# Kernel tuning notes

Hardware: AMD Instinct MI355X
Metric: run time of the kernel (lower is better)

Reference implementation:

```python
import jax, jax.numpy as jnp
import numpy as np

EPS = np.finfo(np.float32).eps
X_DIM, H_DIM, Z_DIM = 256, 1024, 128
T, B = 128, 256

def _lin(key, fan_in, fan_out):
    k1, k2 = jax.random.split(key)
    lim = 1.0 / np.sqrt(fan_in)
    W = jax.random.uniform(k1, (fan_in, fan_out), jnp.float32, -lim, lim)
    b = jax.random.uniform(k2, (fan_out,), jnp.float32, -lim, lim)
    return W, b

def setup_inputs() -> dict:
    key = jax.random.key(0)
    ks = jax.random.split(key, 20)
    inp = {}
    inp['x'] = jax.random.normal(ks[0], (T, B, X_DIM), jnp.float32)
    inp['h'] = jnp.zeros((1, B, H_DIM), jnp.float32)
    inp['eps'] = jax.random.normal(ks[1], (T, B, Z_DIM), jnp.float32)
    inp['Wpx'], inp['bpx'] = _lin(ks[2], X_DIM, H_DIM)
    inp['Wpz'], inp['bpz'] = _lin(ks[3], Z_DIM, H_DIM)
    inp['Wenc'], inp['benc'] = _lin(ks[4], 2 * H_DIM, H_DIM)
    inp['Wem'], inp['bem'] = _lin(ks[5], H_DIM, Z_DIM)
    inp['Wes'], inp['bes'] = _lin(ks[6], H_DIM, Z_DIM)
    inp['Wpr'], inp['bpr'] = _lin(ks[7], H_DIM, H_DIM)
    inp['Wpm'], inp['bpm'] = _lin(ks[8], H_DIM, Z_DIM)
    inp['Wps'], inp['bps'] = _lin(ks[9], H_DIM, Z_DIM)
    inp['Wdec'], inp['bdec'] = _lin(ks[10], 2 * H_DIM, H_DIM)
    inp['Wdm'], inp['bdm'] = _lin(ks[11], H_DIM, X_DIM)
    inp['Wds'], inp['bds'] = _lin(ks[12], H_DIM, X_DIM)
    # GRU (pytorch layout): W_ih [3H, 2H], W_hh [3H, H]
    lim = 1.0 / np.sqrt(H_DIM)
    inp['W_ih'] = jax.random.uniform(ks[13], (3 * H_DIM, 2 * H_DIM), jnp.float32, -lim, lim)
    inp['W_hh'] = jax.random.uniform(ks[14], (3 * H_DIM, H_DIM), jnp.float32, -lim, lim)
    inp['b_ih'] = jax.random.uniform(ks[15], (3 * H_DIM,), jnp.float32, -lim, lim)
    inp['b_hh'] = jax.random.uniform(ks[16], (3 * H_DIM,), jnp.float32, -lim, lim)
    return inp

def reference(x, h, eps, Wpx, bpx, Wpz, bpz, Wenc, benc, Wem, bem, Wes, bes,
              Wpr, bpr, Wpm, bpm, Wps, bps, Wdec, bdec, Wdm, bdm, Wds, bds,
              W_ih, W_hh, b_ih, b_hh):
    relu = jax.nn.relu
    sp = jax.nn.softplus

    def gru_cell(inp, h_prev):
        gi = inp @ W_ih.T + b_ih          # [B, 3H]
        gh = h_prev @ W_hh.T + b_hh       # [B, 3H]
        i_r, i_z, i_n = jnp.split(gi, 3, axis=-1)
        h_r, h_z, h_n = jnp.split(gh, 3, axis=-1)
        r = jax.nn.sigmoid(i_r + h_r)
        u = jax.nn.sigmoid(i_z + h_z)
        n = jnp.tanh(i_n + r * h_n)
        return (1.0 - u) * n + u * h_prev

    def step(h_t, xe):
        x_t, eps_t = xe
        phi_x_t = relu(x_t @ Wpx + bpx)                               # [B,H]
        enc_t = relu(jnp.concatenate([phi_x_t, h_t], axis=1) @ Wenc + benc)
        enc_mean_t = enc_t @ Wem + bem
        enc_std_t = sp(enc_t @ Wes + bes)
        z_t = enc_mean_t + eps_t * enc_std_t                          # reparam
        phi_z_t = relu(z_t @ Wpz + bpz)
        prior_t = relu(h_t @ Wpr + bpr)
        prior_mean_t = prior_t @ Wpm + bpm
        prior_std_t = sp(prior_t @ Wps + bps)
        dec_t = relu(jnp.concatenate([phi_z_t, h_t], axis=1) @ Wdec + bdec)
        dec_mean_t = dec_t @ Wdm + bdm
        dec_std_t = sp(dec_t @ Wds + bds)
        h_next = gru_cell(jnp.concatenate([phi_x_t, phi_z_t], axis=1), h_t)
        kld_t = 0.5 * jnp.sum(2.0 * jnp.log(prior_std_t + EPS) - 2.0 * jnp.log(enc_std_t + EPS)
                              + (enc_std_t ** 2 + (enc_mean_t - prior_mean_t) ** 2) / prior_std_t ** 2 - 1.0)
        nll_t = jnp.sum(jnp.log(dec_std_t + EPS) + 0.5 * jnp.log(2.0 * jnp.pi)
                        + (x_t - dec_mean_t) ** 2 / (2.0 * dec_std_t ** 2))
        return h_next, (enc_mean_t, enc_std_t, dec_mean_t, dec_std_t, kld_t, nll_t)

    h0 = h[0]  # [B, H]
    _, (enc_means, enc_stds, dec_means, dec_stds, klds, nlls) = jax.lax.scan(step, h0, (x, eps))
    kld_loss = jnp.sum(klds)
    nll_loss = jnp.sum(nlls)
    return (kld_loss, nll_loss, enc_means, enc_stds, dec_means, dec_stds)
```

## Files before the change

### kernel.cpp

```cpp
#include <hip/hip_runtime.h>
#include <math.h>
#include <limits.h>

#define T_DIM 128
#define B_DIM 256
#define X_DIMC 256
#define H_DIMC 1024
#define Z_DIMC 128
#define EPSF 1.1920929e-07f
#define HALF_LOG_2PI 0.91893853320467274f
#define NBLK 768
#define NPB (NBLK / 64)

typedef float f32x4 __attribute__((ext_vector_type(4)));
typedef short bf16x8 __attribute__((ext_vector_type(8)));

struct Seg { int n_end; int kbeg; int kend; const float* bias; int act;
             float* of32; int ld32; short* ob16; int ld16; };
struct Segs { Seg s[4]; };

__host__ __device__ static inline Seg dseg(int n_end, int kbeg, int kend,
    const float* bias, int act, float* of32, int ld32, short* ob16, int ld16)
{
    Seg s; s.n_end = n_end; s.kbeg = kbeg; s.kend = kend; s.bias = bias;
    s.act = act; s.of32 = of32; s.ld32 = ld32; s.ob16 = ob16; s.ld16 = ld16;
    return s;
}
__host__ __device__ static inline Seg dsegend()
{ return dseg(INT_MAX, 0, 64, nullptr, 0, nullptr, 0, nullptr, 0); }

__device__ __forceinline__ short f2bf(float f) {
    unsigned u = __builtin_bit_cast(unsigned, f);
    u += 0x7fffu + ((u >> 16) & 1u);
    return (short)(u >> 16);
}
__device__ __forceinline__ float act_apply(float x, int act) {
    if (act == 1) return fmaxf(x, 0.f);
    if (act == 2) return x > 0.f ? x + log1pf(expf(-x)) : log1pf(expf(x));
    return x;
}
__device__ __forceinline__ void gload16(const short* g, short* l) {
    __builtin_amdgcn_global_load_lds(
        (const __attribute__((address_space(1))) void*)g,
        (__attribute__((address_space(3))) void*)l, 16, 0, 0);
}
__device__ __forceinline__ void gload16a(const short* g, short* l) {
    __builtin_amdgcn_global_load_lds(
        (const __attribute__((address_space(1))) void*)g,
        (__attribute__((address_space(3))) void*)l, 16, 0, 17);
}
__device__ __forceinline__ float ldf(const float* p) {
    return __hip_atomic_load(p, __ATOMIC_RELAXED, __HIP_MEMORY_SCOPE_AGENT);
}
__device__ __forceinline__ void stf(float* p, float v) {
    __hip_atomic_store(p, v, __ATOMIC_RELAXED, __HIP_MEMORY_SCOPE_AGENT);
}
__device__ __forceinline__ void sth(short* p, short v) {
    __hip_atomic_store(p, v, __ATOMIC_RELAXED, __HIP_MEMORY_SCOPE_AGENT);
}

__device__ __forceinline__ void gridbar(unsigned* bar, int phase) {
    __syncthreads();
    if (threadIdx.x == 0) {
        asm volatile("s_waitcnt vmcnt(0) lgkmcnt(0)" ::: "memory");
        unsigned* leaf = bar + ((blockIdx.x & 63) << 5);
        unsigned* root = bar + (64 << 5);
        unsigned* gen  = root + 32;
        unsigned old = __hip_atomic_fetch_add(leaf, 1u, __ATOMIC_RELAXED,
                                              __HIP_MEMORY_SCOPE_AGENT);
        if (((old + 1u) % (unsigned)NPB) == 0u) {
            unsigned r = __hip_atomic_fetch_add(root, 1u, __ATOMIC_RELAXED,
                                                __HIP_MEMORY_SCOPE_AGENT);
            if (((r + 1u) & 63u) == 0u)
                __hip_atomic_store(gen, (r + 1u) >> 6, __ATOMIC_RELAXED,
                                   __HIP_MEMORY_SCOPE_AGENT);
        }
        while ((int)__hip_atomic_load(gen, __ATOMIC_RELAXED,
                                      __HIP_MEMORY_SCOPE_AGENT) < phase)
            __builtin_amdgcn_s_sleep(4);
    }
    __syncthreads();
}

__device__ __forceinline__ void gemm_tile(
    short* __restrict__ smem, int bm0, int bn0,
    const short* __restrict__ A0, int lda0,
    const short* __restrict__ A1, int lda1,
    const short* __restrict__ A2, int lda2,
    int ks1, int ks2,
    const short* __restrict__ BT, int ldb, const Segs& segs)
{
    short* As = smem;
    short* Bs = smem + 12288;
    const int tid = threadIdx.x, lane = tid & 63, wid = tid >> 6;
    __syncthreads();
    Seg sg; int n0;
    if      (bn0 < segs.s[0].n_end) { sg = segs.s[0]; n0 = 0; }
    else if (bn0 < segs.s[1].n_end) { sg = segs.s[1]; n0 = segs.s[0].n_end; }
    else if (bn0 < segs.s[2].n_end) { sg = segs.s[2]; n0 = segs.s[1].n_end; }
    else                            { sg = segs.s[3]; n0 = segs.s[2].n_end; }
    const int nit = (sg.kend - sg.kbeg) >> 6;
    const int row8 = lane >> 3;
    const int kc = ((lane & 7) ^ row8) << 3;
    const int r0 = (wid << 4) + row8, r1 = r0 + 8;

    auto srcA = [&](int r, int gk) -> const short* {
        return (gk < ks1) ? A0 + (size_t)(bm0 + r) * lda0 + gk
             : (gk < ks2) ? A1 + (size_t)(bm0 + r) * lda1 + (gk - ks1)
                          : A2 + (size_t)(bm0 + r) * lda2 + (gk - ks2);
    };
    auto stage = [&](int p, int it) {
        const int gk = sg.kbeg + (it << 6) + kc;
        gload16a(srcA(r0, gk), As + p * 4096 + ((wid << 4) + 0) * 64);
        gload16a(srcA(r1, gk), As + p * 4096 + ((wid << 4) + 8) * 64);
        gload16(BT + (size_t)(bn0 + r0) * ldb + gk, Bs + p * 4096 + ((wid << 4) + 0) * 64);
        gload16(BT + (size_t)(bn0 + r1) * ldb + gk, Bs + p * 4096 + ((wid << 4) + 8) * 64);
    };

    const int l15 = lane & 15, lg = lane >> 4;
    const int wm = (wid >> 1) << 5, wn = (wid & 1) << 5;
    const int swz = (l15 & 7) << 3;
    const int c0 = (lg << 3) ^ swz;
    const int c1 = (32 + (lg << 3)) ^ swz;
    f32x4 acc[2][2] = {};

    stage(0, 0);
    if (nit > 1) stage(1, 1);
    if (nit > 2) stage(2, 2);
    int p = 0;
    for (int it = 0; it < nit; ++it) {
        const int rem = nit - 1 - it;
        if (rem >= 2)      asm volatile("s_waitcnt vmcnt(8)" ::: "memory");
        else if (rem == 1) asm volatile("s_waitcnt vmcnt(4)" ::: "memory");
        else               asm volatile("s_waitcnt vmcnt(0)" ::: "memory");
        asm volatile("s_barrier" ::: "memory");
        const short* Ap = As + p * 4096;
        const short* Bp = Bs + p * 4096;
        bf16x8 a00 = *(const bf16x8*)(Ap + (wm + l15) * 64 + c0);
        bf16x8 a01 = *(const bf16x8*)(Ap + (wm + l15) * 64 + c1);
        bf16x8 a10 = *(const bf16x8*)(Ap + (wm + 16 + l15) * 64 + c0);
        bf16x8 a11 = *(const bf16x8*)(Ap + (wm + 16 + l15) * 64 + c1);
        bf16x8 b00 = *(const bf16x8*)(Bp + (wn + l15) * 64 + c0);
        bf16x8 b01 = *(const bf16x8*)(Bp + (wn + l15) * 64 + c1);
        bf16x8 b10 = *(const bf16x8*)(Bp + (wn + 16 + l15) * 64 + c0);
        bf16x8 b11 = *(const bf16x8*)(Bp + (wn + 16 + l15) * 64 + c1);
        acc[0][0] = __builtin_amdgcn_mfma_f32_16x16x32_bf16(a00, b00, acc[0][0], 0, 0, 0);
        acc[0][1] = __builtin_amdgcn_mfma_f32_16x16x32_bf16(a00, b10, acc[0][1], 0, 0, 0);
        acc[1][0] = __builtin_amdgcn_mfma_f32_16x16x32_bf16(a10, b00, acc[1][0], 0, 0, 0);
        acc[1][1] = __builtin_amdgcn_mfma_f32_16x16x32_bf16(a10, b10, acc[1][1], 0, 0, 0);
        acc[0][0] = __builtin_amdgcn_mfma_f32_16x16x32_bf16(a01, b01, acc[0][0], 0, 0, 0);
        acc[0][1] = __builtin_amdgcn_mfma_f32_16x16x32_bf16(a01, b11, acc[0][1], 0, 0, 0);
        acc[1][0] = __builtin_amdgcn_mfma_f32_16x16x32_bf16(a11, b01, acc[1][0], 0, 0, 0);
        acc[1][1] = __builtin_amdgcn_mfma_f32_16x16x32_bf16(a11, b11, acc[1][1], 0, 0, 0);
        if (rem >= 3) {
            asm volatile("s_waitcnt lgkmcnt(0)\n\ts_barrier" ::: "memory");
            stage(p, it + 3);
        }
        p = (p == 2) ? 0 : p + 1;
    }

#pragma unroll
    for (int j = 0; j < 2; ++j) {
        const int gn = bn0 + wn + (j << 4) + l15;
        const int cn = gn - n0;
        const float bv = sg.bias[cn];
#pragma unroll
        for (int i = 0; i < 2; ++i) {
            const int gm0 = bm0 + wm + (i << 4) + (lg << 2);
#pragma unroll
            for (int r = 0; r < 4; ++r) {
                float v = act_apply(acc[i][j][r] + bv, sg.act);
                if (sg.of32) stf(sg.of32 + (size_t)(gm0 + r) * sg.ld32 + cn, v);
                if (sg.ob16) sth(sg.ob16 + (size_t)(gm0 + r) * sg.ld16 + cn, f2bf(v));
            }
        }
    }
}

__device__ __forceinline__ void z_tile(
    short* __restrict__ smem, int bm0, int bn0,
    const float* __restrict__ zm, const float* __restrict__ zs,
    const float* __restrict__ ze,
    const short* __restrict__ BT, const float* __restrict__ bias,
    short* __restrict__ outb)
{
    short* Az = smem;
    short* Bz = smem + 64 * 136;
    const int tid = threadIdx.x, lane = tid & 63, wid = tid >> 6;
    __syncthreads();
    const int r = tid >> 2, c0i = (tid & 3) << 3;
#pragma unroll
    for (int s = 0; s < 4; ++s) {
        const int col = c0i + s * 32;
        const size_t base = (size_t)(bm0 + r) * 128 + col;
        short tmp[8];
#pragma unroll
        for (int q = 0; q < 8; ++q) {
            const float m = ldf(zm + base + q);
            const float sd = ldf(zs + base + q);
            const float e = ze[base + q];
            tmp[q] = f2bf(fmaf(e, sd, m));
        }
        *(bf16x8*)(Az + r * 136 + col) = *(bf16x8*)tmp;
        *(bf16x8*)(Bz + r * 136 + col) =
            *(const bf16x8*)(BT + (size_t)(bn0 + r) * 128 + col);
    }
    __syncthreads();
    const int l15 = lane & 15, lg = lane >> 4;
    const int wm = (wid >> 1) << 5, wn = (wid & 1) << 5;
    f32x4 acc[2][2] = {};
#pragma unroll
    for (int s = 0; s < 4; ++s) {
        bf16x8 af0 = *(const bf16x8*)(Az + (wm + l15) * 136 + (lg << 3) + s * 32);
        bf16x8 af1 = *(const bf16x8*)(Az + (wm + 16 + l15) * 136 + (lg << 3) + s * 32);
        bf16x8 bg0 = *(const bf16x8*)(Bz + (wn + l15) * 136 + (lg << 3) + s * 32);
        bf16x8 bg1 = *(const bf16x8*)(Bz + (wn + 16 + l15) * 136 + (lg << 3) + s * 32);
        acc[0][0] = __builtin_amdgcn_mfma_f32_16x16x32_bf16(af0, bg0, acc[0][0], 0, 0, 0);
        acc[0][1] = __builtin_amdgcn_mfma_f32_16x16x32_bf16(af0, bg1, acc[0][1], 0, 0, 0);
        acc[1][0] = __builtin_amdgcn_mfma_f32_16x16x32_bf16(af1, bg0, acc[1][0], 0, 0, 0);
        acc[1][1] = __builtin_amdgcn_mfma_f32_16x16x32_bf16(af1, bg1, acc[1][1], 0, 0, 0);
    }
#pragma unroll
    for (int j = 0; j < 2; ++j) {
        const int gn = bn0 + wn + (j << 4) + l15;
        const float bv = bias[gn];
#pragma unroll
        for (int i = 0; i < 2; ++i) {
            const int gm0 = bm0 + wm + (i << 4) + (lg << 2);
#pragma unroll
            for (int rr = 0; rr < 4; ++rr) {
                float v = fmaxf(acc[i][j][rr] + bv, 0.f);
                sth(outb + (size_t)(gm0 + rr) * 1024 + gn, f2bf(v));
            }
        }
    }
}

__device__ __forceinline__ void gru_unit(int uid, int tid,
    const float* __restrict__ gi, const float* __restrict__ gh,
    const float* __restrict__ h, float* __restrict__ hn, short* __restrict__ hnb)
{
    const int i = uid * 256 + tid;
    const int b = i >> 10, j = i & (H_DIMC - 1);
    const float* gib = gi + (size_t)b * 3 * H_DIMC;
    const float* ghb = gh + (size_t)b * 3 * H_DIMC;
    const float r = 1.f / (1.f + expf(-(ldf(gib + j) + ldf(ghb + j))));
    const float u = 1.f / (1.f + expf(-(ldf(gib + H_DIMC + j) + ldf(ghb + H_DIMC + j))));
    const float n = tanhf(ldf(gib + 2 * H_DIMC + j) + r * ldf(ghb + 2 * H_DIMC + j));
    const float v = (1.f - u) * n + u * ldf(h + i);
    stf(hn + i, v); sth(hnb + i, f2bf(v));
}

__device__ __forceinline__ void loss_unit(int uid, int tid,
    const float* __restrict__ em, const float* __restrict__ es,
    const float* __restrict__ pm, const float* __restrict__ ps,
    const float* __restrict__ xt, const float* __restrict__ dm,
    const float* __restrict__ ds, float* __restrict__ outp, float* sred)
{
    const int KB = (B_DIM * Z_DIMC) / 256;
    float v; int target;
    if (uid < KB) {
        const int i = uid * 256 + tid;
        const float esv = ldf(es + i), psv = ldf(ps + i);
        const float dmn = ldf(em + i) - ldf(pm + i);
        v = 0.5f * (2.f * logf(psv + EPSF) - 2.f * logf(esv + EPSF) +
                    (esv * esv + dmn * dmn) / (psv * psv) - 1.f);
        target = 0;
    } else {
        const int i = (uid - KB) * 256 + tid;
        const float d = ldf(ds + i);
        const float diff = xt[i] - ldf(dm + i);
        v = logf(d + EPSF) + HALF_LOG_2PI + diff * diff / (2.f * d * d);
        target = 1;
    }
    for (int o = 32; o > 0; o >>= 1) v += __shfl_down(v, o);
    if ((tid & 63) == 0) sred[tid >> 6] = v;
    __syncthreads();
    if (tid == 0) atomicAdd(outp + target, sred[0] + sred[1] + sred[2] + sred[3]);
    __syncthreads();
}

struct PP {
    const short* xb; const float* x; const float* eps;
    const short *WTpx, *WT1, *WT2, *WTpz, *WT4, *WT56;
    const float *bpx, *benc, *bpr, *bhh, *bem, *bes, *bpz, *bdec, *bih,
                *bpm, *bps, *bdm, *bds;
    float *hf0, *hf1; short *hb0, *hb1;
    short *enc_b, *prior_b, *phi_zb, *dec_b;
    short *phiXb, *phiXs;
    float *ghb, *gib, *pmb, *psb;
    float *kld, *em, *es, *dm, *ds;
    unsigned* bar; int big;
};

__global__ __launch_bounds__(256, 3) void vrnn_k(PP p)
{
    __shared__ short smem[24576];
    __shared__ float sred[4];
    const int G = gridDim.x, bid = blockIdx.x, tid = threadIdx.x;
    const int BIGK = 1 << 30;
    int ph = 0;

    Segs sx;
    sx.s[0] = dseg(1024, 0, 256, p.bpx, 1, nullptr, 0, p.big ? p.phiXb : p.phiXs, 1024);
    sx.s[1] = dsegend(); sx.s[2] = dsegend(); sx.s[3] = dsegend();

    if (p.big) {
        for (int u = bid; u < 512 * 16; u += G)
            gemm_tile(smem, (u & 511) << 6, (u >> 9) << 6,
                      p.xb, 256, p.xb, 256, p.xb, 256, BIGK, BIGK,
                      p.WTpx, 256, sx);
        gridbar(p.bar, ++ph);
    }

    for (int t = 0; t < T_DIM; ++t) {
        float* hcur = (t & 1) ? p.hf1 : p.hf0;
        float* hnxt = (t & 1) ? p.hf0 : p.hf1;
        const short* hbc = (t & 1) ? p.hb1 : p.hb0;
        short* hbn = (t & 1) ? p.hb0 : p.hb1;
        const short* phiXt = p.big ? p.phiXb + (size_t)t * B_DIM * H_DIMC : p.phiXs;
        float* em_t = p.em + (size_t)t * B_DIM * Z_DIMC;
        float* es_t = p.es + (size_t)t * B_DIM * Z_DIMC;
        float* dm_t = p.dm + (size_t)t * B_DIM * X_DIMC;
        float* ds_t = p.ds + (size_t)t * B_DIM * X_DIMC;
        const float* eps_t = p.eps + (size_t)t * B_DIM * Z_DIMC;

        if (!p.big) {
            for (int u = bid; u < 64; u += G)
                gemm_tile(smem, (u & 3) << 6, (u >> 2) << 6,
                          p.xb + (size_t)t * B_DIM * X_DIMC, 256,
                          p.xb, 256, p.xb, 256, BIGK, BIGK, p.WTpx, 256, sx);
            gridbar(p.bar, ++ph);
        }
        {
            Segs g1;
            g1.s[0] = dseg(1024, 0, 2048, p.benc, 1, nullptr, 0, p.enc_b, 1024);
            g1.s[1] = dseg(2048, 1024, 2048, p.bpr, 1, nullptr, 0, p.prior_b, 1024);
            g1.s[2] = dseg(5120, 1024, 2048, p.bhh, 0, p.ghb, 3 * H_DIMC, nullptr, 0);
            g1.s[3] = dsegend();
            const int tp = t - 1;
            const int nA = 320 + (t > 0 ? 384 : 0);
            for (int u = bid; u < nA; u += G) {
                if (u < 320)
                    gemm_tile(smem, (u & 3) << 6, (u >> 2) << 6,
                              phiXt, 1024, hbc, 1024, hbc, 1024, 1024, BIGK,
                              p.WT1, 2048, g1);
                else
                    loss_unit(u - 320, tid,
                              p.em + (size_t)tp * B_DIM * Z_DIMC,
                              p.es + (size_t)tp * B_DIM * Z_DIMC,
                              p.pmb, p.psb,
                              p.x + (size_t)tp * B_DIM * X_DIMC,
                              p.dm + (size_t)tp * B_DIM * X_DIMC,
                              p.ds + (size_t)tp * B_DIM * X_DIMC,
                              p.kld, sred);
            }
            gridbar(p.bar, ++ph);
        }
        {
            Segs g2;
            g2.s[0] = dseg(128, 0, 1024, p.bem, 0, em_t, 128, nullptr, 0);
            g2.s[1] = dseg(256, 0, 1024, p.bes, 2, es_t, 128, nullptr, 0);
            g2.s[2] = dsegend(); g2.s[3] = dsegend();
            for (int u = bid; u < 16; u += G)
                gemm_tile(smem, (u & 3) << 6, (u >> 2) << 6,
                          p.enc_b, 1024, p.enc_b, 1024, p.enc_b, 1024, BIGK, BIGK,
                          p.WT2, 1024, g2);
            gridbar(p.bar, ++ph);
        }
        for (int u = bid; u < 64; u += G)
            z_tile(smem, (u & 3) << 6, (u >> 2) << 6,
                   em_t, es_t, eps_t, p.WTpz, p.bpz, p.phi_zb);
        gridbar(p.bar, ++ph);
        {
            Segs g4;
            g4.s[0] = dseg(1024, 1024, 3072, p.bdec, 1, nullptr, 0, p.dec_b, 1024);
            g4.s[1] = dseg(4096, 0, 2048, p.bih, 0, p.gib, 3 * H_DIMC, nullptr, 0);
            g4.s[2] = dsegend(); g4.s[3] = dsegend();
            for (int u = bid; u < 256; u += G)
                gemm_tile(smem, (u & 3) << 6, (u >> 2) << 6,
                          phiXt, 1024, p.phi_zb, 1024, hbc, 1024, 1024, 2048,
                          p.WT4, 3072, g4);
            gridbar(p.bar, ++ph);
        }
        {
            Segs g5;
            g5.s[0] = dseg(128, 0, 1024, p.bpm, 0, p.pmb, 128, nullptr, 0);
            g5.s[1] = dseg(256, 0, 1024, p.bps, 2, p.psb, 128, nullptr, 0);
            g5.s[2] = dseg(512, 1024, 2048, p.bdm, 0, dm_t, 256, nullptr, 0);
            g5.s[3] = dseg(768, 1024, 2048, p.bds, 2, ds_t, 256, nullptr, 0);
            for (int u = bid; u < 48 + 1024; u += G) {
                if (u < 48)
                    gemm_tile(smem, (u & 3) << 6, (u >> 2) << 6,
                              p.prior_b, 1024, p.dec_b, 1024, p.dec_b, 1024,
                              1024, BIGK, p.WT56, 2048, g5);
                else
                    gru_unit(u - 48, tid, p.gib, p.ghb, hcur, hnxt, hbn);
            }
            gridbar(p.bar, ++ph);
        }
    }
    {
        const int tp = T_DIM - 1;
        for (int u = bid; u < 384; u += G)
            loss_unit(u, tid,
                      p.em + (size_t)tp * B_DIM * Z_DIMC,
                      p.es + (size_t)tp * B_DIM * Z_DIMC,
                      p.pmb, p.psb,
                      p.x + (size_t)tp * B_DIM * X_DIMC,
                      p.dm + (size_t)tp * B_DIM * X_DIMC,
                      p.ds + (size_t)tp * B_DIM * X_DIMC,
                      p.kld, sred);
    }
}

__global__ void packT_k(const float* __restrict__ src, int ldsr,
                        short* __restrict__ dst, int ldd, int n0, int k0)
{
    __shared__ float tile[32][33];
    const int bx = blockIdx.x * 32, by = blockIdx.y * 32;
    const int tx = threadIdx.x, ty = threadIdx.y;
    for (int i = ty; i < 32; i += 8)
        tile[i][tx] = src[(size_t)(by + i) * ldsr + bx + tx];
    __syncthreads();
    for (int i = ty; i < 32; i += 8)
        dst[(size_t)(n0 + bx + i) * ldd + k0 + by + tx] = f2bf(tile[tx][i]);
}

__global__ void packD_k(const float* __restrict__ src, int ldsr,
                        short* __restrict__ dst, int ldd, int n0, int k0, int kr)
{
    const int idx = blockIdx.x * 256 + threadIdx.x;
    const int n = idx / kr, k = idx % kr;
    dst[(size_t)(n0 + n) * ldd + k0 + k] = f2bf(src[(size_t)n * ldsr + k]);
}

__global__ void cvtx_k(const float* __restrict__ x, short* __restrict__ xb)
{
    const int i = blockIdx.x * 256 + threadIdx.x;
    float4 v = ((const float4*)x)[i];
    short4 s;
    s.x = f2bf(v.x); s.y = f2bf(v.y); s.z = f2bf(v.z); s.w = f2bf(v.w);
    ((short4*)xb)[i] = s;
}

__global__ void hinit_k(const float* __restrict__ h0, float* __restrict__ hf,
                        short* __restrict__ hb)
{
    const int i = blockIdx.x * 256 + threadIdx.x;
    const float v = h0[i];
    hf[i] = v; hb[i] = f2bf(v);
}

__global__ void init_k(unsigned* bar, float* kn)
{
    for (int i = threadIdx.x; i < 64 * 32 + 64; i += 256) bar[i] = 0u;
    if (threadIdx.x < 2) kn[threadIdx.x] = 0.f;
}

extern "C" void kernel_launch(void* const* d_in, const int* in_sizes, int n_in,
                              void* d_out_v, int out_size, void* d_ws, size_t ws_size,
                              hipStream_t stream)
{
    (void)in_sizes; (void)n_in; (void)out_size;
    const float* x    = (const float*)d_in[0];
    const float* h0   = (const float*)d_in[1];
    const float* eps  = (const float*)d_in[2];
    const float* Wpx  = (const float*)d_in[3];
    const float* bpx  = (const float*)d_in[4];
    const float* Wpz  = (const float*)d_in[5];
    const float* bpz  = (const float*)d_in[6];
    const float* Wenc = (const float*)d_in[7];
    const float* benc = (const float*)d_in[8];
    const float* Wem  = (const float*)d_in[9];
    const float* bem  = (const float*)d_in[10];
    const float* Wes  = (const float*)d_in[11];
    const float* bes  = (const float*)d_in[12];
    const float* Wpr  = (const float*)d_in[13];
    const float* bpr  = (const float*)d_in[14];
    const float* Wpm  = (const float*)d_in[15];
    const float* bpm  = (const float*)d_in[16];
    const float* Wps  = (const float*)d_in[17];
    const float* bps  = (const float*)d_in[18];
    const float* Wdec = (const float*)d_in[19];
    const float* bdec = (const float*)d_in[20];
    const float* Wdm  = (const float*)d_in[21];
    const float* bdm  = (const float*)d_in[22];
    const float* Wds  = (const float*)d_in[23];
    const float* bds  = (const float*)d_in[24];
    const float* W_ih = (const float*)d_in[25];
    const float* W_hh = (const float*)d_in[26];
    const float* b_ih = (const float*)d_in[27];
    const float* b_hh = (const float*)d_in[28];

    float* out = (float*)d_out_v;

    char* wsb = (char*)d_ws;
    size_t off = 0;
    auto takeB = [&](size_t bytes) {
        char* p = wsb + off; off += (bytes + 255) & ~(size_t)255; return p;
    };
    short* WTpx = (short*)takeB((size_t)1024 * 256 * 2);
    short* WT1  = (short*)takeB((size_t)5120 * 2048 * 2);
    short* WT2  = (short*)takeB((size_t)256 * 1024 * 2);
    short* WTpz = (short*)takeB((size_t)1024 * 128 * 2);
    short* WT4  = (short*)takeB((size_t)4096 * 3072 * 2);
    short* WT56 = (short*)takeB((size_t)768 * 2048 * 2);
    short* xb   = (short*)takeB((size_t)T_DIM * B_DIM * X_DIMC * 2);
    float* hf0  = (float*)takeB((size_t)B_DIM * H_DIMC * 4);
    float* hf1  = (float*)takeB((size_t)B_DIM * H_DIMC * 4);
    short* hb0  = (short*)takeB((size_t)B_DIM * H_DIMC * 2);
    short* hb1  = (short*)takeB((size_t)B_DIM * H_DIMC * 2);
    short* enc_b   = (short*)takeB((size_t)B_DIM * H_DIMC * 2);
    short* prior_b = (short*)takeB((size_t)B_DIM * H_DIMC * 2);
    short* phi_zb  = (short*)takeB((size_t)B_DIM * H_DIMC * 2);
    short* dec_b   = (short*)takeB((size_t)B_DIM * H_DIMC * 2);
    float* ghb_ = (float*)takeB((size_t)B_DIM * 3 * H_DIMC * 4);
    float* gib_ = (float*)takeB((size_t)B_DIM * 3 * H_DIMC * 4);
    float* pmb  = (float*)takeB((size_t)B_DIM * Z_DIMC * 4);
    float* psb  = (float*)takeB((size_t)B_DIM * Z_DIMC * 4);
    unsigned* bar = (unsigned*)takeB((64 * 32 + 64) * 4);
    const size_t phiXb_bytes = (size_t)T_DIM * B_DIM * H_DIMC * 2;
    const bool big = (off + phiXb_bytes) <= ws_size;
    short* phiXb = big ? (short*)takeB(phiXb_bytes) : nullptr;
    short* phiXs = big ? nullptr : (short*)takeB((size_t)B_DIM * H_DIMC * 2);

    const dim3 tb(256), pt(32, 8);

    packT_k<<<dim3(32, 8), pt, 0, stream>>>(Wpx, 1024, WTpx, 256, 0, 0);
    packT_k<<<dim3(32, 64), pt, 0, stream>>>(Wenc, 1024, WT1, 2048, 0, 0);
    packT_k<<<dim3(32, 32), pt, 0, stream>>>(Wpr, 1024, WT1, 2048, 1024, 1024);
    packD_k<<<dim3(3072 * 1024 / 256), tb, 0, stream>>>(W_hh, 1024, WT1, 2048, 2048, 1024, 1024);
    packT_k<<<dim3(4, 32), pt, 0, stream>>>(Wem, 128, WT2, 1024, 0, 0);
    packT_k<<<dim3(4, 32), pt, 0, stream>>>(Wes, 128, WT2, 1024, 128, 0);
    packT_k<<<dim3(32, 4), pt, 0, stream>>>(Wpz, 1024, WTpz, 128, 0, 0);
    packT_k<<<dim3(32, 64), pt, 0, stream>>>(Wdec, 1024, WT4, 3072, 0, 1024);
    packD_k<<<dim3(3072 * 2048 / 256), tb, 0, stream>>>(W_ih, 2048, WT4, 3072, 1024, 0, 2048);
    packT_k<<<dim3(4, 32), pt, 0, stream>>>(Wpm, 128, WT56, 2048, 0, 0);
    packT_k<<<dim3(4, 32), pt, 0, stream>>>(Wps, 128, WT56, 2048, 128, 0);
    packT_k<<<dim3(8, 32), pt, 0, stream>>>(Wdm, 256, WT56, 2048, 256, 1024);
    packT_k<<<dim3(8, 32), pt, 0, stream>>>(Wds, 256, WT56, 2048, 512, 1024);

    cvtx_k<<<dim3((size_t)T_DIM * B_DIM * X_DIMC / 4 / 256), tb, 0, stream>>>(x, xb);
    hinit_k<<<dim3(B_DIM * H_DIMC / 256), tb, 0, stream>>>(h0, hf0, hb0);
    init_k<<<1, 256, 0, stream>>>(bar, out);

    PP p;
    p.xb = xb; p.x = x; p.eps = eps;
    p.WTpx = WTpx; p.WT1 = WT1; p.WT2 = WT2; p.WTpz = WTpz; p.WT4 = WT4; p.WT56 = WT56;
    p.bpx = bpx; p.benc = benc; p.bpr = bpr; p.bhh = b_hh; p.bem = bem; p.bes = bes;
    p.bpz = bpz; p.bdec = bdec; p.bih = b_ih; p.bpm = bpm; p.bps = bps;
    p.bdm = bdm; p.bds = bds;
    p.hf0 = hf0; p.hf1 = hf1; p.hb0 = hb0; p.hb1 = hb1;
    p.enc_b = enc_b; p.prior_b = prior_b; p.phi_zb = phi_zb; p.dec_b = dec_b;
    p.phiXb = phiXb; p.phiXs = phiXs;
    p.ghb = ghb_; p.gib = gib_; p.pmb = pmb; p.psb = psb;
    p.kld = out; p.em = out + 2;
    p.es = p.em + (size_t)T_DIM * B_DIM * Z_DIMC;
    p.dm = p.es + (size_t)T_DIM * B_DIM * Z_DIMC;
    p.ds = p.dm + (size_t)T_DIM * B_DIM * X_DIMC;
    p.bar = bar; p.big = big ? 1 : 0;

    vrnn_k<<<dim3(NBLK), tb, 0, stream>>>(p);
}
```

Before: 15.51 ms.

## Widen GEMM tiles to 64x128, halve grid, vectorize epilogues and elementwise units

The persistent kernel's GEMM tile grows from 64x64 to 64x128 with a double-buffered rather than triple-buffered LDS pipeline. The block count drops from 768 to 384, which should make every grid barrier cheaper. Epilogues now stage accumulators through LDS so they can be written as dwordx4 stores with packed bf16. The GRU, z and loss units switch to 4-wide coherent vector loads via inline asm. The trade-off is fewer tiles per phase, so each small per-step GEMM gets less parallelism, and the shallower prefetch may expose more load latency.

```diff
diff --git a/kernel.cpp b/kernel.cpp
--- a/kernel.cpp
+++ b/kernel.cpp
@@ -9,11 +9,13 @@
 #define Z_DIMC 128
 #define EPSF 1.1920929e-07f
 #define HALF_LOG_2PI 0.91893853320467274f
-#define NBLK 768
+#define NBLK 384
 #define NPB (NBLK / 64)
 
 typedef float f32x4 __attribute__((ext_vector_type(4)));
 typedef short bf16x8 __attribute__((ext_vector_type(8)));
+typedef int int4v __attribute__((ext_vector_type(4)));
+typedef int int2v __attribute__((ext_vector_type(2)));
 
 struct Seg { int n_end; int kbeg; int kend; const float* bias; int act;
              float* of32; int ld32; short* ob16; int ld16; };
@@ -34,6 +36,10 @@
     u += 0x7fffu + ((u >> 16) & 1u);
     return (short)(u >> 16);
 }
+__device__ __forceinline__ int packbf2(float a, float b) {
+    return (int)((((unsigned)(unsigned short)f2bf(b)) << 16) |
+                 (unsigned)(unsigned short)f2bf(a));
+}
 __device__ __forceinline__ float act_apply(float x, int act) {
     if (act == 1) return fmaxf(x, 0.f);
     if (act == 2) return x > 0.f ? x + log1pf(expf(-x)) : log1pf(expf(x));
@@ -49,20 +55,43 @@
         (const __attribute__((address_space(1))) void*)g,
         (__attribute__((address_space(3))) void*)l, 16, 0, 17);
 }
-__device__ __forceinline__ float ldf(const float* p) {
-    return __hip_atomic_load(p, __ATOMIC_RELAXED, __HIP_MEMORY_SCOPE_AGENT);
-}
-__device__ __forceinline__ void stf(float* p, float v) {
-    __hip_atomic_store(p, v, __ATOMIC_RELAXED, __HIP_MEMORY_SCOPE_AGENT);
-}
-__device__ __forceinline__ void sth(short* p, short v) {
-    __hip_atomic_store(p, v, __ATOMIC_RELAXED, __HIP_MEMORY_SCOPE_AGENT);
+__device__ __forceinline__ void ldg4x2(const float* p0, const float* p1,
+                                       f32x4& a, f32x4& b) {
+    asm volatile(
+        "global_load_dwordx4 %0, %2, off sc0 sc1\n\t"
+        "global_load_dwordx4 %1, %3, off sc0 sc1\n\t"
+        "s_waitcnt vmcnt(0)"
+        : "=&v"(a), "=&v"(b) : "v"(p0), "v"(p1) : "memory");
+}
+__device__ __forceinline__ void ldg4x4(const float* p0, const float* p1,
+                                       const float* p2, const float* p3,
+                                       f32x4& a, f32x4& b, f32x4& c, f32x4& d) {
+    asm volatile(
+        "global_load_dwordx4 %0, %4, off sc0 sc1\n\t"
+        "global_load_dwordx4 %1, %5, off sc0 sc1\n\t"
+        "global_load_dwordx4 %2, %6, off sc0 sc1\n\t"
+        "global_load_dwordx4 %3, %7, off sc0 sc1\n\t"
+        "s_waitcnt vmcnt(0)"
+        : "=&v"(a), "=&v"(b), "=&v"(c), "=&v"(d)
+        : "v"(p0), "v"(p1), "v"(p2), "v"(p3) : "memory");
+}
+__device__ __forceinline__ void stg4f(float* p, f32x4 v) {
+    asm volatile("global_store_dwordx4 %0, %1, off sc0 sc1"
+                 :: "v"(p), "v"(v) : "memory");
+}
+__device__ __forceinline__ void stg4i(short* p, int4v v) {
+    asm volatile("global_store_dwordx4 %0, %1, off sc0 sc1"
+                 :: "v"(p), "v"(v) : "memory");
+}
+__device__ __forceinline__ void stg2i(short* p, int2v v) {
+    asm volatile("global_store_dwordx2 %0, %1, off sc0 sc1"
+                 :: "v"(p), "v"(v) : "memory");
 }
 
 __device__ __forceinline__ void gridbar(unsigned* bar, int phase) {
+    asm volatile("s_waitcnt vmcnt(0)" ::: "memory");
     __syncthreads();
     if (threadIdx.x == 0) {
-        asm volatile("s_waitcnt vmcnt(0) lgkmcnt(0)" ::: "memory");
         unsigned* leaf = bar + ((blockIdx.x & 63) << 5);
         unsigned* root = bar + (64 << 5);
         unsigned* gen  = root + 32;
@@ -91,7 +120,7 @@
     const short* __restrict__ BT, int ldb, const Segs& segs)
 {
     short* As = smem;
-    short* Bs = smem + 12288;
+    short* Bs = smem + 8192;
     const int tid = threadIdx.x, lane = tid & 63, wid = tid >> 6;
     __syncthreads();
     Seg sg; int n0;
@@ -102,7 +131,8 @@
     const int nit = (sg.kend - sg.kbeg) >> 6;
     const int row8 = lane >> 3;
     const int kc = ((lane & 7) ^ row8) << 3;
-    const int r0 = (wid << 4) + row8, r1 = r0 + 8;
+    const int ar = (wid << 4) + row8;
+    const int br = (wid << 5) + row8;
 
     auto srcA = [&](int r, int gk) -> const short* {
         return (gk < ks1) ? A0 + (size_t)(bm0 + r) * lda0 + gk
@@ -111,68 +141,91 @@
     };
     auto stage = [&](int p, int it) {
         const int gk = sg.kbeg + (it << 6) + kc;
-        gload16a(srcA(r0, gk), As + p * 4096 + ((wid << 4) + 0) * 64);
-        gload16a(srcA(r1, gk), As + p * 4096 + ((wid << 4) + 8) * 64);
-        gload16(BT + (size_t)(bn0 + r0) * ldb + gk, Bs + p * 4096 + ((wid << 4) + 0) * 64);
-        gload16(BT + (size_t)(bn0 + r1) * ldb + gk, Bs + p * 4096 + ((wid << 4) + 8) * 64);
+        gload16a(srcA(ar, gk),     As + p * 4096 + ((wid << 4) + 0) * 64);
+        gload16a(srcA(ar + 8, gk), As + p * 4096 + ((wid << 4) + 8) * 64);
+        gload16(BT + (size_t)(bn0 + br) * ldb + gk,      Bs + p * 8192 + ((wid << 5) + 0) * 64);
+        gload16(BT + (size_t)(bn0 + br + 8) * ldb + gk,  Bs + p * 8192 + ((wid << 5) + 8) * 64);
+        gload16(BT + (size_t)(bn0 + br + 16) * ldb + gk, Bs + p * 8192 + ((wid << 5) + 16) * 64);
+        gload16(BT + (size_t)(bn0 + br + 24) * ldb + gk, Bs + p * 8192 + ((wid << 5) + 24) * 64);
     };
 
     const int l15 = lane & 15, lg = lane >> 4;
-    const int wm = (wid >> 1) << 5, wn = (wid & 1) << 5;
+    const int wm = (wid >> 1) << 5, wn = (wid & 1) << 6;
     const int swz = (l15 & 7) << 3;
-    const int c0 = (lg << 3) ^ swz;
-    const int c1 = (32 + (lg << 3)) ^ swz;
-    f32x4 acc[2][2] = {};
+    const int cA = (lg << 3) ^ swz;
+    const int cB = (32 + (lg << 3)) ^ swz;
+    f32x4 acc[2][4] = {};
 
     stage(0, 0);
     if (nit > 1) stage(1, 1);
-    if (nit > 2) stage(2, 2);
     int p = 0;
     for (int it = 0; it < nit; ++it) {
         const int rem = nit - 1 - it;
-        if (rem >= 2)      asm volatile("s_waitcnt vmcnt(8)" ::: "memory");
-        else if (rem == 1) asm volatile("s_waitcnt vmcnt(4)" ::: "memory");
-        else               asm volatile("s_waitcnt vmcnt(0)" ::: "memory");
+        if (rem >= 1) asm volatile("s_waitcnt vmcnt(6)" ::: "memory");
+        else          asm volatile("s_waitcnt vmcnt(0)" ::: "memory");
         asm volatile("s_barrier" ::: "memory");
         const short* Ap = As + p * 4096;
-        const short* Bp = Bs + p * 4096;
-        bf16x8 a00 = *(const bf16x8*)(Ap + (wm + l15) * 64 + c0);
-        bf16x8 a01 = *(const bf16x8*)(Ap + (wm + l15) * 64 + c1);
-        bf16x8 a10 = *(const bf16x8*)(Ap + (wm + 16 + l15) * 64 + c0);
-        bf16x8 a11 = *(const bf16x8*)(Ap + (wm + 16 + l15) * 64 + c1);
-        bf16x8 b00 = *(const bf16x8*)(Bp + (wn + l15) * 64 + c0);
-        bf16x8 b01 = *(const bf16x8*)(Bp + (wn + l15) * 64 + c1);
-        bf16x8 b10 = *(const bf16x8*)(Bp + (wn + 16 + l15) * 64 + c0);
-        bf16x8 b11 = *(const bf16x8*)(Bp + (wn + 16 + l15) * 64 + c1);
-        acc[0][0] = __builtin_amdgcn_mfma_f32_16x16x32_bf16(a00, b00, acc[0][0], 0, 0, 0);
-        acc[0][1] = __builtin_amdgcn_mfma_f32_16x16x32_bf16(a00, b10, acc[0][1], 0, 0, 0);
-        acc[1][0] = __builtin_amdgcn_mfma_f32_16x16x32_bf16(a10, b00, acc[1][0], 0, 0, 0);
-        acc[1][1] = __builtin_amdgcn_mfma_f32_16x16x32_bf16(a10, b10, acc[1][1], 0, 0, 0);
-        acc[0][0] = __builtin_amdgcn_mfma_f32_16x16x32_bf16(a01, b01, acc[0][0], 0, 0, 0);
-        acc[0][1] = __builtin_amdgcn_mfma_f32_16x16x32_bf16(a01, b11, acc[0][1], 0, 0, 0);
-        acc[1][0] = __builtin_amdgcn_mfma_f32_16x16x32_bf16(a11, b01, acc[1][0], 0, 0, 0);
-        acc[1][1] = __builtin_amdgcn_mfma_f32_16x16x32_bf16(a11, b11, acc[1][1], 0, 0, 0);
-        if (rem >= 3) {
+        const short* Bp = Bs + p * 8192;
+#pragma unroll
+        for (int h = 0; h < 2; ++h) {
+            const int cc = h ? cB : cA;
+            bf16x8 a0 = *(const bf16x8*)(Ap + (wm + l15) * 64 + cc);
+            bf16x8 a1 = *(const bf16x8*)(Ap + (wm + 16 + l15) * 64 + cc);
+            bf16x8 b0 = *(const bf16x8*)(Bp + (wn + l15) * 64 + cc);
+            bf16x8 b1 = *(const bf16x8*)(Bp + (wn + 16 + l15) * 64 + cc);
+            bf16x8 b2 = *(const bf16x8*)(Bp + (wn + 32 + l15) * 64 + cc);
+            bf16x8 b3 = *(const bf16x8*)(Bp + (wn + 48 + l15) * 64 + cc);
+            acc[0][0] = __builtin_amdgcn_mfma_f32_16x16x32_bf16(a0, b0, acc[0][0], 0, 0, 0);
+            acc[0][1] = __builtin_amdgcn_mfma_f32_16x16x32_bf16(a0, b1, acc[0][1], 0, 0, 0);
+            acc[0][2] = __builtin_amdgcn_mfma_f32_16x16x32_bf16(a0, b2, acc[0][2], 0, 0, 0);
+            acc[0][3] = __builtin_amdgcn_mfma_f32_16x16x32_bf16(a0, b3, acc[0][3], 0, 0, 0);
+            acc[1][0] = __builtin_amdgcn_mfma_f32_16x16x32_bf16(a1, b0, acc[1][0], 0, 0, 0);
+            acc[1][1] = __builtin_amdgcn_mfma_f32_16x16x32_bf16(a1, b1, acc[1][1], 0, 0, 0);
+            acc[1][2] = __builtin_amdgcn_mfma_f32_16x16x32_bf16(a1, b2, acc[1][2], 0, 0, 0);
+            acc[1][3] = __builtin_amdgcn_mfma_f32_16x16x32_bf16(a1, b3, acc[1][3], 0, 0, 0);
+        }
+        if (rem >= 2) {
             asm volatile("s_waitcnt lgkmcnt(0)\n\ts_barrier" ::: "memory");
-            stage(p, it + 3);
-        }
-        p = (p == 2) ? 0 : p + 1;
-    }
-
-#pragma unroll
-    for (int j = 0; j < 2; ++j) {
-        const int gn = bn0 + wn + (j << 4) + l15;
-        const int cn = gn - n0;
-        const float bv = sg.bias[cn];
-#pragma unroll
-        for (int i = 0; i < 2; ++i) {
-            const int gm0 = bm0 + wm + (i << 4) + (lg << 2);
-#pragma unroll
-            for (int r = 0; r < 4; ++r) {
-                float v = act_apply(acc[i][j][r] + bv, sg.act);
-                if (sg.of32) stf(sg.of32 + (size_t)(gm0 + r) * sg.ld32 + cn, v);
-                if (sg.ob16) sth(sg.ob16 + (size_t)(gm0 + r) * sg.ld16 + cn, f2bf(v));
-            }
+            stage(p, it + 2);
+        }
+        p ^= 1;
+    }
+
+    __syncthreads();
+    float* bounce = (float*)smem;
+#pragma unroll
+    for (int i = 0; i < 2; ++i)
+#pragma unroll
+        for (int j = 0; j < 4; ++j)
+#pragma unroll
+            for (int r = 0; r < 4; ++r)
+                bounce[(wm + i * 16 + (lg << 2) + r) * 132 + wn + j * 16 + l15] =
+                    acc[i][j][r];
+    __syncthreads();
+    const int brow = tid >> 2, bc0 = (tid & 3) << 5;
+    const int gm = bm0 + brow;
+    const int cn0 = bn0 + bc0 - n0;
+#pragma unroll
+    for (int c = 0; c < 4; ++c) {
+        const int cn = cn0 + (c << 3);
+        const float* bp = bounce + brow * 132 + bc0 + (c << 3);
+        const f32x4 bb0 = *(const f32x4*)(sg.bias + cn);
+        const f32x4 bb1 = *(const f32x4*)(sg.bias + cn + 4);
+        f32x4 v0, v1;
+#pragma unroll
+        for (int q = 0; q < 4; ++q) {
+            v0[q] = act_apply(bp[q] + bb0[q], sg.act);
+            v1[q] = act_apply(bp[q + 4] + bb1[q], sg.act);
+        }
+        if (sg.of32) {
+            float* qp = sg.of32 + (size_t)gm * sg.ld32 + cn;
+            stg4f(qp, v0); stg4f(qp + 4, v1);
+        }
+        if (sg.ob16) {
+            int4v pk;
+            pk[0] = packbf2(v0[0], v0[1]); pk[1] = packbf2(v0[2], v0[3]);
+            pk[2] = packbf2(v1[0], v1[1]); pk[3] = packbf2(v1[2], v1[3]);
+            stg4i(sg.ob16 + (size_t)gm * sg.ld16 + cn, pk);
         }
     }
 }
@@ -185,21 +238,23 @@
     short* __restrict__ outb)
 {
     short* Az = smem;
-    short* Bz = smem + 64 * 136;
+    short* Bz = smem + 8704;
     const int tid = threadIdx.x, lane = tid & 63, wid = tid >> 6;
     __syncthreads();
-    const int r = tid >> 2, c0i = (tid & 3) << 3;
+    const int r = tid >> 2, c8 = (tid & 3) << 3;
 #pragma unroll
     for (int s = 0; s < 4; ++s) {
-        const int col = c0i + s * 32;
+        const int col = c8 + s * 32;
         const size_t base = (size_t)(bm0 + r) * 128 + col;
+        f32x4 m0, m1, s0, s1;
+        ldg4x4(zm + base, zm + base + 4, zs + base, zs + base + 4, m0, m1, s0, s1);
+        const f32x4 e0 = *(const f32x4*)(ze + base);
+        const f32x4 e1 = *(const f32x4*)(ze + base + 4);
         short tmp[8];
 #pragma unroll
-        for (int q = 0; q < 8; ++q) {
-            const float m = ldf(zm + base + q);
-            const float sd = ldf(zs + base + q);
-            const float e = ze[base + q];
-            tmp[q] = f2bf(fmaf(e, sd, m));
+        for (int q = 0; q < 4; ++q) {
+            tmp[q]     = f2bf(fmaf(e0[q], s0[q], m0[q]));
+            tmp[q + 4] = f2bf(fmaf(e1[q], s1[q], m1[q]));
         }
         *(bf16x8*)(Az + r * 136 + col) = *(bf16x8*)tmp;
         *(bf16x8*)(Bz + r * 136 + col) =
@@ -220,19 +275,30 @@
         acc[1][0] = __builtin_amdgcn_mfma_f32_16x16x32_bf16(af1, bg0, acc[1][0], 0, 0, 0);
         acc[1][1] = __builtin_amdgcn_mfma_f32_16x16x32_bf16(af1, bg1, acc[1][1], 0, 0, 0);
     }
-#pragma unroll
-    for (int j = 0; j < 2; ++j) {
-        const int gn = bn0 + wn + (j << 4) + l15;
-        const float bv = bias[gn];
-#pragma unroll
-        for (int i = 0; i < 2; ++i) {
-            const int gm0 = bm0 + wm + (i << 4) + (lg << 2);
-#pragma unroll
-            for (int rr = 0; rr < 4; ++rr) {
-                float v = fmaxf(acc[i][j][rr] + bv, 0.f);
-                sth(outb + (size_t)(gm0 + rr) * 1024 + gn, f2bf(v));
-            }
-        }
+    __syncthreads();
+    float* bounce = (float*)smem;
+#pragma unroll
+    for (int j = 0; j < 2; ++j)
+#pragma unroll
+        for (int i = 0; i < 2; ++i)
+#pragma unroll
+            for (int rr = 0; rr < 4; ++rr)
+                bounce[(wm + i * 16 + (lg << 2) + rr) * 68 + wn + j * 16 + l15] =
+                    acc[i][j][rr];
+    __syncthreads();
+    const int brow = tid >> 2, bc0 = (tid & 3) << 4;
+    const int gm = bm0 + brow, gn = bn0 + bc0;
+#pragma unroll
+    for (int c = 0; c < 2; ++c) {
+        const float* bp = bounce + brow * 68 + bc0 + (c << 3);
+        const f32x4 bb0 = *(const f32x4*)(bias + gn + (c << 3));
+        const f32x4 bb1 = *(const f32x4*)(bias + gn + (c << 3) + 4);
+        int4v pk;
+        pk[0] = packbf2(fmaxf(bp[0] + bb0[0], 0.f), fmaxf(bp[1] + bb0[1], 0.f));
+        pk[1] = packbf2(fmaxf(bp[2] + bb0[2], 0.f), fmaxf(bp[3] + bb0[3], 0.f));
+        pk[2] = packbf2(fmaxf(bp[4] + bb1[0], 0.f), fmaxf(bp[5] + bb1[1], 0.f));
+        pk[3] = packbf2(fmaxf(bp[6] + bb1[2], 0.f), fmaxf(bp[7] + bb1[3], 0.f));
+        stg4i(outb + (size_t)gm * 1024 + gn + (c << 3), pk);
     }
 }
 
@@ -240,15 +306,39 @@
     const float* __restrict__ gi, const float* __restrict__ gh,
     const float* __restrict__ h, float* __restrict__ hn, short* __restrict__ hnb)
 {
-    const int i = uid * 256 + tid;
-    const int b = i >> 10, j = i & (H_DIMC - 1);
-    const float* gib = gi + (size_t)b * 3 * H_DIMC;
-    const float* ghb = gh + (size_t)b * 3 * H_DIMC;
-    const float r = 1.f / (1.f + expf(-(ldf(gib + j) + ldf(ghb + j))));
-    const float u = 1.f / (1.f + expf(-(ldf(gib + H_DIMC + j) + ldf(ghb + H_DIMC + j))));
-    const float n = tanhf(ldf(gib + 2 * H_DIMC + j) + r * ldf(ghb + 2 * H_DIMC + j));
-    const float v = (1.f - u) * n + u * ldf(h + i);
-    stf(hn + i, v); sth(hnb + i, f2bf(v));
+    const int i = (uid * 256 + tid) << 2;
+    const int b = i >> 10, j = i & 1023;
+    const float* pgi = gi + (size_t)b * 3072 + j;
+    const float* pgh = gh + (size_t)b * 3072 + j;
+    f32x4 ir, iz, in_, hr, hz, hn_, hv;
+    asm volatile(
+        "global_load_dwordx4 %0, %7, off sc0 sc1\n\t"
+        "global_load_dwordx4 %1, %8, off sc0 sc1\n\t"
+        "global_load_dwordx4 %2, %9, off sc0 sc1\n\t"
+        "global_load_dwordx4 %3, %10, off sc0 sc1\n\t"
+        "global_load_dwordx4 %4, %11, off sc0 sc1\n\t"
+        "global_load_dwordx4 %5, %12, off sc0 sc1\n\t"
+        "global_load_dwordx4 %6, %13, off sc0 sc1\n\t"
+        "s_waitcnt vmcnt(0)"
+        : "=&v"(ir), "=&v"(iz), "=&v"(in_), "=&v"(hr), "=&v"(hz), "=&v"(hn_), "=&v"(hv)
+        : "v"(pgi), "v"(pgi + 1024), "v"(pgi + 2048),
+          "v"(pgh), "v"(pgh + 1024), "v"(pgh + 2048), "v"(h + i)
+        : "memory");
+    f32x4 out;
+    short hb4[4];
+#pragma unroll
+    for (int q = 0; q < 4; ++q) {
+        const float rr = 1.f / (1.f + expf(-(ir[q] + hr[q])));
+        const float uu = 1.f / (1.f + expf(-(iz[q] + hz[q])));
+        const float nn = tanhf(in_[q] + rr * hn_[q]);
+        const float v = (1.f - uu) * nn + uu * hv[q];
+        out[q] = v; hb4[q] = f2bf(v);
+    }
+    stg4f(hn + i, out);
+    int2v pk;
+    pk[0] = (int)((((unsigned)(unsigned short)hb4[1]) << 16) | (unsigned)(unsigned short)hb4[0]);
+    pk[1] = (int)((((unsigned)(unsigned short)hb4[3]) << 16) | (unsigned)(unsigned short)hb4[2]);
+    stg2i(hnb + i, pk);
 }
 
 __device__ __forceinline__ void loss_unit(int uid, int tid,
@@ -257,20 +347,28 @@
     const float* __restrict__ xt, const float* __restrict__ dm,
     const float* __restrict__ ds, float* __restrict__ outp, float* sred)
 {
-    const int KB = (B_DIM * Z_DIMC) / 256;
-    float v; int target;
-    if (uid < KB) {
-        const int i = uid * 256 + tid;
-        const float esv = ldf(es + i), psv = ldf(ps + i);
-        const float dmn = ldf(em + i) - ldf(pm + i);
-        v = 0.5f * (2.f * logf(psv + EPSF) - 2.f * logf(esv + EPSF) +
-                    (esv * esv + dmn * dmn) / (psv * psv) - 1.f);
+    float v = 0.f; int target;
+    if (uid < 32) {
+        const int i = (uid * 256 + tid) << 2;
+        f32x4 a, b, c, d;
+        ldg4x4(em + i, es + i, pm + i, ps + i, a, b, c, d);
+#pragma unroll
+        for (int q = 0; q < 4; ++q) {
+            const float dmn = a[q] - c[q];
+            v += 0.5f * (2.f * logf(d[q] + EPSF) - 2.f * logf(b[q] + EPSF) +
+                         (b[q] * b[q] + dmn * dmn) / (d[q] * d[q]) - 1.f);
+        }
         target = 0;
     } else {
-        const int i = (uid - KB) * 256 + tid;
-        const float d = ldf(ds + i);
-        const float diff = xt[i] - ldf(dm + i);
-        v = logf(d + EPSF) + HALF_LOG_2PI + diff * diff / (2.f * d * d);
+        const int i = ((uid - 32) * 256 + tid) << 2;
+        f32x4 m, sd;
+        ldg4x2(dm + i, ds + i, m, sd);
+        const f32x4 xv = *(const f32x4*)(xt + i);
+#pragma unroll
+        for (int q = 0; q < 4; ++q) {
+            const float diff = xv[q] - m[q];
+            v += logf(sd[q] + EPSF) + HALF_LOG_2PI + diff * diff / (2.f * sd[q] * sd[q]);
+        }
         target = 1;
     }
     for (int o = 32; o > 0; o >>= 1) v += __shfl_down(v, o);
@@ -293,7 +391,7 @@
     unsigned* bar; int big;
 };
 
-__global__ __launch_bounds__(256, 3) void vrnn_k(PP p)
+__global__ __launch_bounds__(256, 2) void vrnn_k(PP p)
 {
     __shared__ short smem[24576];
     __shared__ float sred[4];
@@ -306,8 +404,8 @@
     sx.s[1] = dsegend(); sx.s[2] = dsegend(); sx.s[3] = dsegend();
 
     if (p.big) {
-        for (int u = bid; u < 512 * 16; u += G)
-            gemm_tile(smem, (u & 511) << 6, (u >> 9) << 6,
+        for (int u = bid; u < 512 * 8; u += G)
+            gemm_tile(smem, (u & 511) << 6, (u >> 9) << 7,
                       p.xb, 256, p.xb, 256, p.xb, 256, BIGK, BIGK,
                       p.WTpx, 256, sx);
         gridbar(p.bar, ++ph);
@@ -326,8 +424,8 @@
         const float* eps_t = p.eps + (size_t)t * B_DIM * Z_DIMC;
 
         if (!p.big) {
-            for (int u = bid; u < 64; u += G)
-                gemm_tile(smem, (u & 3) << 6, (u >> 2) << 6,
+            for (int u = bid; u < 32; u += G)
+                gemm_tile(smem, (u & 3) << 6, (u >> 2) << 7,
                           p.xb + (size_t)t * B_DIM * X_DIMC, 256,
                           p.xb, 256, p.xb, 256, BIGK, BIGK, p.WTpx, 256, sx);
             gridbar(p.bar, ++ph);
@@ -339,14 +437,14 @@
             g1.s[2] = dseg(5120, 1024, 2048, p.bhh, 0, p.ghb, 3 * H_DIMC, nullptr, 0);
             g1.s[3] = dsegend();
             const int tp = t - 1;
-            const int nA = 320 + (t > 0 ? 384 : 0);
+            const int nA = 160 + (t > 0 ? 96 : 0);
             for (int u = bid; u < nA; u += G) {
-                if (u < 320)
-                    gemm_tile(smem, (u & 3) << 6, (u >> 2) << 6,
+                if (u < 160)
+                    gemm_tile(smem, (u & 3) << 6, (u >> 2) << 7,
                               phiXt, 1024, hbc, 1024, hbc, 1024, 1024, BIGK,
                               p.WT1, 2048, g1);
                 else
-                    loss_unit(u - 320, tid,
+                    loss_unit(u - 160, tid,
                               p.em + (size_t)tp * B_DIM * Z_DIMC,
                               p.es + (size_t)tp * B_DIM * Z_DIMC,
                               p.pmb, p.psb,
@@ -362,8 +460,8 @@
             g2.s[0] = dseg(128, 0, 1024, p.bem, 0, em_t, 128, nullptr, 0);
             g2.s[1] = dseg(256, 0, 1024, p.bes, 2, es_t, 128, nullptr, 0);
             g2.s[2] = dsegend(); g2.s[3] = dsegend();
-            for (int u = bid; u < 16; u += G)
-                gemm_tile(smem, (u & 3) << 6, (u >> 2) << 6,
+            for (int u = bid; u < 8; u += G)
+                gemm_tile(smem, (u & 3) << 6, (u >> 2) << 7,
                           p.enc_b, 1024, p.enc_b, 1024, p.enc_b, 1024, BIGK, BIGK,
                           p.WT2, 1024, g2);
             gridbar(p.bar, ++ph);
@@ -377,8 +475,8 @@
             g4.s[0] = dseg(1024, 1024, 3072, p.bdec, 1, nullptr, 0, p.dec_b, 1024);
             g4.s[1] = dseg(4096, 0, 2048, p.bih, 0, p.gib, 3 * H_DIMC, nullptr, 0);
             g4.s[2] = dsegend(); g4.s[3] = dsegend();
-            for (int u = bid; u < 256; u += G)
-                gemm_tile(smem, (u & 3) << 6, (u >> 2) << 6,
+            for (int u = bid; u < 128; u += G)
+                gemm_tile(smem, (u & 3) << 6, (u >> 2) << 7,
                           phiXt, 1024, p.phi_zb, 1024, hbc, 1024, 1024, 2048,
                           p.WT4, 3072, g4);
             gridbar(p.bar, ++ph);
@@ -389,20 +487,20 @@
             g5.s[1] = dseg(256, 0, 1024, p.bps, 2, p.psb, 128, nullptr, 0);
             g5.s[2] = dseg(512, 1024, 2048, p.bdm, 0, dm_t, 256, nullptr, 0);
             g5.s[3] = dseg(768, 1024, 2048, p.bds, 2, ds_t, 256, nullptr, 0);
-            for (int u = bid; u < 48 + 1024; u += G) {
-                if (u < 48)
-                    gemm_tile(smem, (u & 3) << 6, (u >> 2) << 6,
+            for (int u = bid; u < 24 + 256; u += G) {
+                if (u < 24)
+                    gemm_tile(smem, (u & 3) << 6, (u >> 2) << 7,
                               p.prior_b, 1024, p.dec_b, 1024, p.dec_b, 1024,
                               1024, BIGK, p.WT56, 2048, g5);
                 else
-                    gru_unit(u - 48, tid, p.gib, p.ghb, hcur, hnxt, hbn);
+                    gru_unit(u - 24, tid, p.gib, p.ghb, hcur, hnxt, hbn);
             }
             gridbar(p.bar, ++ph);
         }
     }
     {
         const int tp = T_DIM - 1;
-        for (int u = bid; u < 384; u += G)
+        for (int u = bid; u < 96; u += G)
             loss_unit(u, tid,
                       p.em + (size_t)tp * B_DIM * Z_DIMC,
                       p.es + (size_t)tp * B_DIM * Z_DIMC,
```

Measured after the change: 20.45 ms. 31.8% more time.
